# Performance work log

Hardware: AMD Instinct MI355X
Metric: run time of the kernel (lower is better)

The kernel has to match this reference:

```python
import jax, jax.numpy as jnp
import numpy as np

NEG_BIG = -9e15


def setup_inputs() -> dict:
    key = jax.random.key(0)
    k1, k2, k3, k4 = jax.random.split(key, 4)
    B, N, F_in, F_out = 8, 2048, 512, 256
    x = jax.random.normal(k1, (B, N, F_in), dtype=jnp.float32)
    adj = jax.random.randint(k2, (B, N, N), 0, 2, dtype=jnp.int32)
    W = jax.random.normal(k3, (F_in, F_out), dtype=jnp.float32) * (1.414 / np.sqrt(F_in))
    a = jax.random.normal(k4, (2 * F_out, 1), dtype=jnp.float32) * 0.1
    return {"x": x, "adj": adj, "W": W, "a": a}


def reference(x, adj, W, a):
    # x: [B,N,Fin], adj: [B,N,N] int mask, W: [Fin,Fout], a: [2*Fout,1]
    alpha = 0.2  # LeakyReLU negative slope
    F_out = W.shape[1]
    h = jnp.einsum('bnf,fo->bno', x, W)              # [B,N,Fout]
    a1 = a[:F_out, 0]                                # [Fout]
    a2 = a[F_out:, 0]                                # [Fout]
    # e_ij = LeakyReLU([h_i || h_j] . a) = LeakyReLU(h_i.a1 + h_j.a2)
    f = h @ a1                                       # [B,N]
    g = h @ a2                                       # [B,N]
    e = jax.nn.leaky_relu(f[:, :, None] + g[:, None, :], negative_slope=alpha)  # [B,N,N]
    e = jnp.where(adj > 0, e, NEG_BIG)
    attention = jax.nn.softmax(e, axis=2)            # row-wise over neighbors j
    h_prime = jnp.einsum('bij,bjo->bio', attention, h)  # [B,N,Fout]
    return jax.nn.elu(h_prime)                       # concat=True path
```

## Files before the change

### kernel.cpp

```cpp
#include <hip/hip_runtime.h>
#include <math.h>

#define BATCH 8
#define NN    2048
#define FIN   512
#define FOUT  256
#define NEG_BIG -9000000000000000.0f

typedef __attribute__((ext_vector_type(8))) short bf16x8;
typedef __attribute__((ext_vector_type(4))) float f32x4;

__device__ __forceinline__ unsigned short f2bf(float x) {
    unsigned u = __float_as_uint(x);
    u = (u + 0x7FFF + ((u >> 16) & 1)) >> 16;
    return (unsigned short)u;
}
__device__ __forceinline__ float bf2f(unsigned short h) {
    return __uint_as_float(((unsigned)h) << 16);
}
__device__ __forceinline__ void gload_lds16(const void* g, void* l) {
    __builtin_amdgcn_global_load_lds((const __attribute__((address_space(1))) void*)g,
                                     (__attribute__((address_space(3))) void*)l,
                                     16, 0, 0);
}

__global__ __launch_bounds__(256) void wt_prep(const float* __restrict__ W,
                                               unsigned short* __restrict__ Wt_hi,
                                               unsigned short* __restrict__ Wt_lo) {
    const int tg = blockIdx.x * 256 + threadIdx.x;
    const int n  = tg >> 7;
    const int k4 = (tg & 127) * 4;
    unsigned short h[4], lo[4];
    #pragma unroll
    for (int i = 0; i < 4; i++) {
        const float v = W[(size_t)(k4 + i) * FOUT + n];
        h[i]  = f2bf(v);
        lo[i] = f2bf(v - bf2f(h[i]));
    }
    uint2 ph, pl;
    ph.x = h[0]  | ((unsigned)h[1]  << 16); ph.y = h[2]  | ((unsigned)h[3]  << 16);
    pl.x = lo[0] | ((unsigned)lo[1] << 16); pl.y = lo[2] | ((unsigned)lo[3] << 16);
    *(uint2*)(Wt_hi + (size_t)n * FIN + k4) = ph;
    *(uint2*)(Wt_lo + (size_t)n * FIN + k4) = pl;
}

__global__ __launch_bounds__(256, 2) void gemm_xw(const float* __restrict__ x,
        const unsigned short* __restrict__ Wt_hi,
        const unsigned short* __restrict__ Wt_lo,
        unsigned short* __restrict__ ht_hi,
        unsigned short* __restrict__ ht_lo) {
    __shared__ unsigned short As_hi[128][40];
    __shared__ unsigned short As_lo[128][40];
    __shared__ __attribute__((aligned(16))) unsigned short Tr[64][136];
    const int t  = threadIdx.x;
    const int m0 = (blockIdx.x >> 2) * 128;
    const int n0 = (blockIdx.x & 3) * 64;
    const int l  = t & 63, w = t >> 6;
    const int wr = w >> 1, wc = w & 1;
    const int lr = l & 15, lk = l >> 4;

    f32x4 acc[4][2];
    #pragma unroll
    for (int mt = 0; mt < 4; mt++)
        #pragma unroll
        for (int nt = 0; nt < 2; nt++) acc[mt][nt] = (f32x4){0.f,0.f,0.f,0.f};

    for (int k0 = 0; k0 < FIN; k0 += 32) {
        float4 xv[4];
        #pragma unroll
        for (int r = 0; r < 4; r++) {
            const int fidx = t + 256*r, m = fidx >> 3, kq = fidx & 7;
            xv[r] = *(const float4*)(x + (size_t)(m0 + m) * FIN + k0 + kq*4);
        }
        bf16x8 bh[2], bl[2];
        #pragma unroll
        for (int nt = 0; nt < 2; nt++) {
            const size_t off = (size_t)(n0 + wc*32 + nt*16 + lr) * FIN + k0 + lk*8;
            bh[nt] = *(const bf16x8*)(Wt_hi + off);
            bl[nt] = *(const bf16x8*)(Wt_lo + off);
        }
        __syncthreads();
        #pragma unroll
        for (int r = 0; r < 4; r++) {
            const int fidx = t + 256*r, m = fidx >> 3, kq = fidx & 7;
            const float vv[4] = {xv[r].x, xv[r].y, xv[r].z, xv[r].w};
            unsigned short h[4], lo[4];
            #pragma unroll
            for (int i = 0; i < 4; i++) { h[i] = f2bf(vv[i]); lo[i] = f2bf(vv[i] - bf2f(h[i])); }
            uint2 ph, pl;
            ph.x = h[0]  | ((unsigned)h[1]  << 16); ph.y = h[2]  | ((unsigned)h[3]  << 16);
            pl.x = lo[0] | ((unsigned)lo[1] << 16); pl.y = lo[2] | ((unsigned)lo[3] << 16);
            *(uint2*)&As_hi[m][kq*4] = ph;
            *(uint2*)&As_lo[m][kq*4] = pl;
        }
        __syncthreads();
        bf16x8 ah[4], al[4];
        #pragma unroll
        for (int mt = 0; mt < 4; mt++) {
            const int row = wr*64 + mt*16 + lr;
            ah[mt] = *(const bf16x8*)&As_hi[row][lk*8];
            al[mt] = *(const bf16x8*)&As_lo[row][lk*8];
        }
        #pragma unroll
        for (int nt = 0; nt < 2; nt++)
            #pragma unroll
            for (int mt = 0; mt < 4; mt++)
                acc[mt][nt] = __builtin_amdgcn_mfma_f32_16x16x32_bf16(ah[mt], bh[nt], acc[mt][nt], 0, 0, 0);
        #pragma unroll
        for (int nt = 0; nt < 2; nt++)
            #pragma unroll
            for (int mt = 0; mt < 4; mt++)
                acc[mt][nt] = __builtin_amdgcn_mfma_f32_16x16x32_bf16(ah[mt], bl[nt], acc[mt][nt], 0, 0, 0);
        #pragma unroll
        for (int nt = 0; nt < 2; nt++)
            #pragma unroll
            for (int mt = 0; mt < 4; mt++)
                acc[mt][nt] = __builtin_amdgcn_mfma_f32_16x16x32_bf16(al[mt], bh[nt], acc[mt][nt], 0, 0, 0);
    }

    const int bb  = m0 >> 11;
    const int jj0 = m0 & 2047;
    for (int pass = 0; pass < 2; pass++) {
        #pragma unroll
        for (int mt = 0; mt < 4; mt++)
            #pragma unroll
            for (int nt = 0; nt < 2; nt++) {
                const int nl = wc*32 + nt*16 + lr;
                const int ml = wr*64 + mt*16 + lk*4;
                const float vv[4] = {acc[mt][nt].x, acc[mt][nt].y, acc[mt][nt].z, acc[mt][nt].w};
                unsigned short s[4];
                #pragma unroll
                for (int r = 0; r < 4; r++) {
                    const unsigned short hh = f2bf(vv[r]);
                    s[r] = pass ? f2bf(vv[r] - bf2f(hh)) : hh;
                }
                *(unsigned*)&Tr[nl][ml]     = s[0] | ((unsigned)s[1] << 16);
                *(unsigned*)&Tr[nl][ml + 2] = s[2] | ((unsigned)s[3] << 16);
            }
        __syncthreads();
        unsigned short* dst = pass ? ht_lo : ht_hi;
        #pragma unroll
        for (int q = 0; q < 4; q++) {
            const int idx = t + 256*q, row = idx >> 4, c = idx & 15;
            *(uint4*)(dst + ((size_t)(bb * FOUT + n0 + row)) * NN + jj0 + c*8) =
                *(const uint4*)&Tr[row][c*8];
        }
        __syncthreads();
    }
}

__global__ __launch_bounds__(256) void fg2(const unsigned short* __restrict__ ht_hi,
                                           const unsigned short* __restrict__ ht_lo,
                                           const float* __restrict__ a,
                                           float* __restrict__ f, float* __restrict__ g) {
    const int lane  = threadIdx.x & 63;
    const int chunk = blockIdx.x * 4 + (threadIdx.x >> 6);
    const int b  = chunk >> 5;
    const int jw = (chunk & 31) * 64 + lane;
    const size_t base = (size_t)b * FOUT * NN + jw;
    float fs = 0.f, gs = 0.f;
    #pragma unroll 4
    for (int n = 0; n < FOUT; n++) {
        const float hv = bf2f(ht_hi[base + (size_t)n * NN]) + bf2f(ht_lo[base + (size_t)n * NN]);
        fs = fmaf(hv, a[n], fs);
        gs = fmaf(hv, a[FOUT + n], gs);
    }
    f[b * NN + jw] = fs;
    g[b * NN + jw] = gs;
}

__global__ __launch_bounds__(512, 1) void gat_attn(
        const unsigned short* __restrict__ ht_hi,
        const unsigned short* __restrict__ ht_lo,
        const int* __restrict__ adj,
        const float* __restrict__ f, const float* __restrict__ g,
        float* __restrict__ out) {
    __shared__ __attribute__((aligned(16))) unsigned short Hs_hi[256*64];
    __shared__ __attribute__((aligned(16))) unsigned short Hs_lo[256*64];
    __shared__ __attribute__((aligned(16))) unsigned short Ps_hi[64*64];
    __shared__ __attribute__((aligned(16))) unsigned short Ps_lo[64*64];
    __shared__ __attribute__((aligned(16))) float m_s[64];
    __shared__ __attribute__((aligned(16))) float l_s[64];
    __shared__ __attribute__((aligned(16))) float fac_s[64];

    const int b  = blockIdx.x & 7;
    const int i0 = (blockIdx.x >> 3) * 64;
    const int t  = threadIdx.x;
    const int w  = t >> 6, l = t & 63;
    const int lr = l & 15, lk = l >> 4;
    const int wr = w >> 2, wc = w & 3;
    const int ar = t >> 3, jg = t & 7;

    const float fi = f[b * NN + i0 + ar];
    if (t < 64) { m_s[t] = -INFINITY; l_s[t] = 0.f; }

    f32x4 acc[2][4];
    #pragma unroll
    for (int mt = 0; mt < 2; mt++)
        #pragma unroll
        for (int nt = 0; nt < 4; nt++) acc[mt][nt] = (f32x4){0.f,0.f,0.f,0.f};

    const unsigned short* hb_hi = ht_hi + (size_t)b * FOUT * NN;
    const unsigned short* hb_lo = ht_lo + (size_t)b * FOUT * NN;
    const size_t arow = ((size_t)b * NN + i0 + ar) * NN + jg * 8;
    const float* grow = g + b * NN + jg * 8;

    int4   adjA = *(const int4*)(adj + arow);
    int4   adjB = *(const int4*)(adj + arow + 4);
    float4 gA   = *(const float4*)(grow);
    float4 gB   = *(const float4*)(grow + 4);

    const int sidx = w * 4;

    for (int jt = 0; jt < 32; jt++) {
        __syncthreads();

        const int j0 = jt * 64;
        #pragma unroll
        for (int q = 0; q < 4; q++) {
            const int idx = (sidx + q) * 64 + l;
            const int n = idx >> 3, c = idx & 7;
            const int cc = c ^ (n & 7);
            const size_t go = (size_t)n * NN + j0 + cc * 8;
            gload_lds16(hb_hi + go, &Hs_hi[(sidx + q) * 512]);
            gload_lds16(hb_lo + go, &Hs_lo[(sidx + q) * 512]);
        }

        {
            float s[8];
            {
                const float v0 = fi + gA.x, v1 = fi + gA.y, v2 = fi + gA.z, v3 = fi + gA.w;
                const float v4 = fi + gB.x, v5 = fi + gB.y, v6 = fi + gB.z, v7 = fi + gB.w;
                s[0] = adjA.x > 0 ? (v0 > 0.f ? v0 : 0.2f*v0) : NEG_BIG;
                s[1] = adjA.y > 0 ? (v1 > 0.f ? v1 : 0.2f*v1) : NEG_BIG;
                s[2] = adjA.z > 0 ? (v2 > 0.f ? v2 : 0.2f*v2) : NEG_BIG;
                s[3] = adjA.w > 0 ? (v3 > 0.f ? v3 : 0.2f*v3) : NEG_BIG;
                s[4] = adjB.x > 0 ? (v4 > 0.f ? v4 : 0.2f*v4) : NEG_BIG;
                s[5] = adjB.y > 0 ? (v5 > 0.f ? v5 : 0.2f*v5) : NEG_BIG;
                s[6] = adjB.z > 0 ? (v6 > 0.f ? v6 : 0.2f*v6) : NEG_BIG;
                s[7] = adjB.w > 0 ? (v7 > 0.f ? v7 : 0.2f*v7) : NEG_BIG;
            }
            float mloc = s[0];
            #pragma unroll
            for (int e = 1; e < 8; e++) mloc = fmaxf(mloc, s[e]);
            mloc = fmaxf(mloc, __shfl_xor(mloc, 1));
            mloc = fmaxf(mloc, __shfl_xor(mloc, 2));
            mloc = fmaxf(mloc, __shfl_xor(mloc, 4));
            const float m_old = m_s[ar];
            const float m_new = fmaxf(m_old, mloc);
            float p[8], rs = 0.f;
            #pragma unroll
            for (int e = 0; e < 8; e++) { p[e] = __expf(s[e] - m_new); rs += p[e]; }
            rs += __shfl_xor(rs, 1);
            rs += __shfl_xor(rs, 2);
            rs += __shfl_xor(rs, 4);
            if (jg == 0) {
                const float fac = __expf(m_old - m_new);
                fac_s[ar] = fac;
                l_s[ar]   = l_s[ar] * fac + rs;
                m_s[ar]   = m_new;
            }
            unsigned ph[4], pl[4];
            #pragma unroll
            for (int e = 0; e < 8; e += 2) {
                const unsigned short h0 = f2bf(p[e]),   h1 = f2bf(p[e+1]);
                const unsigned short q0 = f2bf(p[e] - bf2f(h0));
                const unsigned short q1 = f2bf(p[e+1] - bf2f(h1));
                ph[e >> 1] = h0 | ((unsigned)h1 << 16);
                pl[e >> 1] = q0 | ((unsigned)q1 << 16);
            }
            const int cs = (jg ^ (ar & 7)) * 8;
            *(uint4*)&Ps_hi[ar * 64 + cs] = make_uint4(ph[0], ph[1], ph[2], ph[3]);
            *(uint4*)&Ps_lo[ar * 64 + cs] = make_uint4(pl[0], pl[1], pl[2], pl[3]);
        }
        __syncthreads();

        if (jt + 1 < 32) {
            const size_t o = (size_t)(jt + 1) * 64;
            adjA = *(const int4*)(adj + arow + o);
            adjB = *(const int4*)(adj + arow + o + 4);
            gA   = *(const float4*)(grow + o);
            gB   = *(const float4*)(grow + o + 4);
        }

        #pragma unroll
        for (int mt = 0; mt < 2; mt++) {
            const f32x4 fac4 = *(const f32x4*)&fac_s[wr*32 + mt*16 + lk*4];
            #pragma unroll
            for (int nt = 0; nt < 4; nt++) acc[mt][nt] *= fac4;
        }
        #pragma unroll
        for (int kt = 0; kt < 2; kt++) {
            bf16x8 ah[2], al[2], bh[4], bl[4];
            #pragma unroll
            for (int mt = 0; mt < 2; mt++) {
                const int row = wr*32 + mt*16 + lr;
                const int cs  = ((kt*4 + lk) ^ (row & 7)) * 8;
                ah[mt] = *(const bf16x8*)&Ps_hi[row * 64 + cs];
                al[mt] = *(const bf16x8*)&Ps_lo[row * 64 + cs];
            }
            #pragma unroll
            for (int nt = 0; nt < 4; nt++) {
                const int n  = wc*64 + nt*16 + lr;
                const int cs = ((kt*4 + lk) ^ (n & 7)) * 8;
                bh[nt] = *(const bf16x8*)&Hs_hi[n * 64 + cs];
                bl[nt] = *(const bf16x8*)&Hs_lo[n * 64 + cs];
            }
            #pragma unroll
            for (int nt = 0; nt < 4; nt++)
                #pragma unroll
                for (int mt = 0; mt < 2; mt++)
                    acc[mt][nt] = __builtin_amdgcn_mfma_f32_16x16x32_bf16(ah[mt], bh[nt], acc[mt][nt], 0, 0, 0);
            #pragma unroll
            for (int nt = 0; nt < 4; nt++)
                #pragma unroll
                for (int mt = 0; mt < 2; mt++)
                    acc[mt][nt] = __builtin_amdgcn_mfma_f32_16x16x32_bf16(ah[mt], bl[nt], acc[mt][nt], 0, 0, 0);
            #pragma unroll
            for (int nt = 0; nt < 4; nt++)
                #pragma unroll
                for (int mt = 0; mt < 2; mt++)
                    acc[mt][nt] = __builtin_amdgcn_mfma_f32_16x16x32_bf16(al[mt], bh[nt], acc[mt][nt], 0, 0, 0);
        }
    }

    __syncthreads();
    #pragma unroll
    for (int mt = 0; mt < 2; mt++) {
        const f32x4 lv = *(const f32x4*)&l_s[wr*32 + mt*16 + lk*4];
        const float linv[4] = {1.f/lv.x, 1.f/lv.y, 1.f/lv.z, 1.f/lv.w};
        #pragma unroll
        for (int nt = 0; nt < 4; nt++) {
            const int n = wc*64 + nt*16 + lr;
            const float av[4] = {acc[mt][nt].x, acc[mt][nt].y, acc[mt][nt].z, acc[mt][nt].w};
            #pragma unroll
            for (int r = 0; r < 4; r++) {
                float v = av[r] * linv[r];
                v = v > 0.f ? v : (__expf(v) - 1.f);
                out[((size_t)(b * NN + i0 + wr*32 + mt*16 + lk*4 + r)) * FOUT + n] = v;
            }
        }
    }
}

extern "C" void kernel_launch(void* const* d_in, const int* in_sizes, int n_in,
                              void* d_out, int out_size, void* d_ws, size_t ws_size,
                              hipStream_t stream) {
    const float* x   = (const float*)d_in[0];
    const int*   adj = (const int*)  d_in[1];
    const float* W   = (const float*)d_in[2];
    const float* a   = (const float*)d_in[3];
    float* outp = (float*)d_out;

    char* ws = (char*)d_ws;
    unsigned short* ht_hi = (unsigned short*)ws;                       ws += (size_t)BATCH*FOUT*NN*2;
    unsigned short* ht_lo = (unsigned short*)ws;                       ws += (size_t)BATCH*FOUT*NN*2;
    unsigned short* Wt_hi = (unsigned short*)ws;                       ws += (size_t)FOUT*FIN*2;
    unsigned short* Wt_lo = (unsigned short*)ws;                       ws += (size_t)FOUT*FIN*2;
    float* f = (float*)ws;                                             ws += (size_t)BATCH*NN*4;
    float* g = (float*)ws;

    wt_prep <<<128, 256, 0, stream>>>(W, Wt_hi, Wt_lo);
    gemm_xw <<<512, 256, 0, stream>>>(x, Wt_hi, Wt_lo, ht_hi, ht_lo);
    fg2     <<<64,  256, 0, stream>>>(ht_hi, ht_lo, a, f, g);
    gat_attn<<<256, 512, 0, stream>>>(ht_hi, ht_lo, adj, f, g, outp);
}
```

Before: 320.5 us.

## Double-buffer H tiles in attention, pre-swizzle W to fragment layout, split fg2 reduction

The attention kernel now keeps the H tiles in two LDS buffers and issues the next tile's async global-to-LDS loads before the softmax of the current tile. It keeps the running max and sum in registers instead of shared memory, uses custom lgkmcnt barriers, and raises wave priority around the MFMA block. W is pre-arranged in MFMA fragment order so gemm_xw reads it with contiguous per-lane loads. fg2 splits the feature reduction across four waves and launches four times as many blocks. Each change targets latency hiding or load efficiency, at the cost of twice the H-tile LDS footprint and more complex synchronization.

```diff
diff --git a/kernel.cpp b/kernel.cpp
--- a/kernel.cpp
+++ b/kernel.cpp
@@ -1,4 +1,5 @@
 #include <hip/hip_runtime.h>
+#include <hip/hip_bf16.h>
 #include <math.h>
 
 #define BATCH 8
@@ -11,9 +12,7 @@
 typedef __attribute__((ext_vector_type(4))) float f32x4;
 
 __device__ __forceinline__ unsigned short f2bf(float x) {
-    unsigned u = __float_as_uint(x);
-    u = (u + 0x7FFF + ((u >> 16) & 1)) >> 16;
-    return (unsigned short)u;
+    return __bfloat16_as_ushort(__float2bfloat16(x));
 }
 __device__ __forceinline__ float bf2f(unsigned short h) {
     return __uint_as_float(((unsigned)h) << 16);
@@ -23,10 +22,15 @@
                                      (__attribute__((address_space(3))) void*)l,
                                      16, 0, 0);
 }
+__device__ __forceinline__ void lds_barrier() {
+    asm volatile("s_waitcnt lgkmcnt(0)" ::: "memory");
+    __builtin_amdgcn_s_barrier();
+    asm volatile("" ::: "memory");
+}
 
 __global__ __launch_bounds__(256) void wt_prep(const float* __restrict__ W,
-                                               unsigned short* __restrict__ Wt_hi,
-                                               unsigned short* __restrict__ Wt_lo) {
+                                               unsigned short* __restrict__ Wtf_hi,
+                                               unsigned short* __restrict__ Wtf_lo) {
     const int tg = blockIdx.x * 256 + threadIdx.x;
     const int n  = tg >> 7;
     const int k4 = (tg & 127) * 4;
@@ -37,16 +41,20 @@
         h[i]  = f2bf(v);
         lo[i] = f2bf(v - bf2f(h[i]));
     }
+    const int ktile = k4 >> 5;
+    const int ntile = n >> 4;
+    const int lane  = ((k4 >> 3) & 3) * 16 + (n & 15);
+    const size_t daddr = ((size_t)(ktile * 16 + ntile) * 64 + lane) * 8 + (k4 & 7);
     uint2 ph, pl;
     ph.x = h[0]  | ((unsigned)h[1]  << 16); ph.y = h[2]  | ((unsigned)h[3]  << 16);
     pl.x = lo[0] | ((unsigned)lo[1] << 16); pl.y = lo[2] | ((unsigned)lo[3] << 16);
-    *(uint2*)(Wt_hi + (size_t)n * FIN + k4) = ph;
-    *(uint2*)(Wt_lo + (size_t)n * FIN + k4) = pl;
+    *(uint2*)(Wtf_hi + daddr) = ph;
+    *(uint2*)(Wtf_lo + daddr) = pl;
 }
 
 __global__ __launch_bounds__(256, 2) void gemm_xw(const float* __restrict__ x,
-        const unsigned short* __restrict__ Wt_hi,
-        const unsigned short* __restrict__ Wt_lo,
+        const unsigned short* __restrict__ Wtf_hi,
+        const unsigned short* __restrict__ Wtf_lo,
         unsigned short* __restrict__ ht_hi,
         unsigned short* __restrict__ ht_lo) {
     __shared__ unsigned short As_hi[128][40];
@@ -73,11 +81,11 @@
             xv[r] = *(const float4*)(x + (size_t)(m0 + m) * FIN + k0 + kq*4);
         }
         bf16x8 bh[2], bl[2];
+        const size_t fb = ((size_t)((k0 >> 5) * 16 + (n0 >> 4) + wc*2) * 64 + l) * 8;
         #pragma unroll
         for (int nt = 0; nt < 2; nt++) {
-            const size_t off = (size_t)(n0 + wc*32 + nt*16 + lr) * FIN + k0 + lk*8;
-            bh[nt] = *(const bf16x8*)(Wt_hi + off);
-            bl[nt] = *(const bf16x8*)(Wt_lo + off);
+            bh[nt] = *(const bf16x8*)(Wtf_hi + fb + (size_t)nt * 512);
+            bl[nt] = *(const bf16x8*)(Wtf_lo + fb + (size_t)nt * 512);
         }
         __syncthreads();
         #pragma unroll
@@ -153,20 +161,25 @@
                                            const unsigned short* __restrict__ ht_lo,
                                            const float* __restrict__ a,
                                            float* __restrict__ f, float* __restrict__ g) {
-    const int lane  = threadIdx.x & 63;
-    const int chunk = blockIdx.x * 4 + (threadIdx.x >> 6);
+    __shared__ float Fp[4][64], Gp[4][64];
+    const int lane = threadIdx.x & 63, wv = threadIdx.x >> 6;
+    const int chunk = blockIdx.x;
     const int b  = chunk >> 5;
     const int jw = (chunk & 31) * 64 + lane;
     const size_t base = (size_t)b * FOUT * NN + jw;
     float fs = 0.f, gs = 0.f;
     #pragma unroll 4
-    for (int n = 0; n < FOUT; n++) {
+    for (int n = wv*64; n < wv*64 + 64; n++) {
         const float hv = bf2f(ht_hi[base + (size_t)n * NN]) + bf2f(ht_lo[base + (size_t)n * NN]);
         fs = fmaf(hv, a[n], fs);
         gs = fmaf(hv, a[FOUT + n], gs);
     }
-    f[b * NN + jw] = fs;
-    g[b * NN + jw] = gs;
+    Fp[wv][lane] = fs; Gp[wv][lane] = gs;
+    __syncthreads();
+    if (wv == 0) {
+        f[b * NN + jw] = Fp[0][lane] + Fp[1][lane] + Fp[2][lane] + Fp[3][lane];
+        g[b * NN + jw] = Gp[0][lane] + Gp[1][lane] + Gp[2][lane] + Gp[3][lane];
+    }
 }
 
 __global__ __launch_bounds__(512, 1) void gat_attn(
@@ -175,13 +188,12 @@
         const int* __restrict__ adj,
         const float* __restrict__ f, const float* __restrict__ g,
         float* __restrict__ out) {
-    __shared__ __attribute__((aligned(16))) unsigned short Hs_hi[256*64];
-    __shared__ __attribute__((aligned(16))) unsigned short Hs_lo[256*64];
-    __shared__ __attribute__((aligned(16))) unsigned short Ps_hi[64*64];
-    __shared__ __attribute__((aligned(16))) unsigned short Ps_lo[64*64];
-    __shared__ __attribute__((aligned(16))) float m_s[64];
+    __shared__ __attribute__((aligned(16))) unsigned short Hs_hi[2][16384];
+    __shared__ __attribute__((aligned(16))) unsigned short Hs_lo[2][16384];
+    __shared__ __attribute__((aligned(16))) unsigned short Ps_hi[4096];
+    __shared__ __attribute__((aligned(16))) unsigned short Ps_lo[4096];
+    __shared__ __attribute__((aligned(16))) float fac_s[64];
     __shared__ __attribute__((aligned(16))) float l_s[64];
-    __shared__ __attribute__((aligned(16))) float fac_s[64];
 
     const int b  = blockIdx.x & 7;
     const int i0 = (blockIdx.x >> 3) * 64;
@@ -191,97 +203,95 @@
     const int wr = w >> 2, wc = w & 3;
     const int ar = t >> 3, jg = t & 7;
 
-    const float fi = f[b * NN + i0 + ar];
-    if (t < 64) { m_s[t] = -INFINITY; l_s[t] = 0.f; }
-
-    f32x4 acc[2][4];
-    #pragma unroll
-    for (int mt = 0; mt < 2; mt++)
-        #pragma unroll
-        for (int nt = 0; nt < 4; nt++) acc[mt][nt] = (f32x4){0.f,0.f,0.f,0.f};
-
     const unsigned short* hb_hi = ht_hi + (size_t)b * FOUT * NN;
     const unsigned short* hb_lo = ht_lo + (size_t)b * FOUT * NN;
-    const size_t arow = ((size_t)b * NN + i0 + ar) * NN + jg * 8;
-    const float* grow = g + b * NN + jg * 8;
-
-    int4   adjA = *(const int4*)(adj + arow);
-    int4   adjB = *(const int4*)(adj + arow + 4);
-    float4 gA   = *(const float4*)(grow);
-    float4 gB   = *(const float4*)(grow + 4);
-
-    const int sidx = w * 4;
-
-    for (int jt = 0; jt < 32; jt++) {
-        __syncthreads();
-
-        const int j0 = jt * 64;
+    const int*   adjr = adj + ((size_t)(b * NN + i0 + ar)) * NN + jg * 8;
+    const float* gb   = g + b * NN + jg * 8;
+    const float  fi   = f[b * NN + i0 + ar];
+
+    float m_r = -INFINITY, l_r = 0.f;
+    f32x4 acc[2][4] = {};
+    const int slot = w * 4;
+
+    int4 a0v, a1v; float4 g0v, g1v;
+
+    auto STAGE = [&](int jt) {
+        const int buf = jt & 1, j0 = jt * 64;
         #pragma unroll
         for (int q = 0; q < 4; q++) {
-            const int idx = (sidx + q) * 64 + l;
+            const int idx = (slot + q) * 64 + l;
             const int n = idx >> 3, c = idx & 7;
             const int cc = c ^ (n & 7);
             const size_t go = (size_t)n * NN + j0 + cc * 8;
-            gload_lds16(hb_hi + go, &Hs_hi[(sidx + q) * 512]);
-            gload_lds16(hb_lo + go, &Hs_lo[(sidx + q) * 512]);
-        }
+            gload_lds16(hb_hi + go, &Hs_hi[buf][(slot + q) * 512]);
+            gload_lds16(hb_lo + go, &Hs_lo[buf][(slot + q) * 512]);
+        }
+    };
+    auto LOADAG = [&](int jt) {
+        const size_t jo = (size_t)jt * 64;
+        a0v = *(const int4*)(adjr + jo);
+        a1v = *(const int4*)(adjr + jo + 4);
+        g0v = *(const float4*)(gb + jo);
+        g1v = *(const float4*)(gb + jo + 4);
+    };
+
+    STAGE(0);
+    asm volatile("" ::: "memory");
+    LOADAG(0);
+
+    for (int jt = 0; jt < 32; jt++) {
+        const int buf = jt & 1;
+        if (jt + 1 < 32) STAGE(jt + 1);
+        asm volatile("" ::: "memory");
 
         {
-            float s[8];
+            float p[8];
             {
-                const float v0 = fi + gA.x, v1 = fi + gA.y, v2 = fi + gA.z, v3 = fi + gA.w;
-                const float v4 = fi + gB.x, v5 = fi + gB.y, v6 = fi + gB.z, v7 = fi + gB.w;
-                s[0] = adjA.x > 0 ? (v0 > 0.f ? v0 : 0.2f*v0) : NEG_BIG;
-                s[1] = adjA.y > 0 ? (v1 > 0.f ? v1 : 0.2f*v1) : NEG_BIG;
-                s[2] = adjA.z > 0 ? (v2 > 0.f ? v2 : 0.2f*v2) : NEG_BIG;
-                s[3] = adjA.w > 0 ? (v3 > 0.f ? v3 : 0.2f*v3) : NEG_BIG;
-                s[4] = adjB.x > 0 ? (v4 > 0.f ? v4 : 0.2f*v4) : NEG_BIG;
-                s[5] = adjB.y > 0 ? (v5 > 0.f ? v5 : 0.2f*v5) : NEG_BIG;
-                s[6] = adjB.z > 0 ? (v6 > 0.f ? v6 : 0.2f*v6) : NEG_BIG;
-                s[7] = adjB.w > 0 ? (v7 > 0.f ? v7 : 0.2f*v7) : NEG_BIG;
-            }
-            float mloc = s[0];
-            #pragma unroll
-            for (int e = 1; e < 8; e++) mloc = fmaxf(mloc, s[e]);
+                const float v0 = fi + g0v.x, v1 = fi + g0v.y, v2 = fi + g0v.z, v3 = fi + g0v.w;
+                const float v4 = fi + g1v.x, v5 = fi + g1v.y, v6 = fi + g1v.z, v7 = fi + g1v.w;
+                p[0] = a0v.x > 0 ? (v0 > 0.f ? v0 : 0.2f*v0) : NEG_BIG;
+                p[1] = a0v.y > 0 ? (v1 > 0.f ? v1 : 0.2f*v1) : NEG_BIG;
+                p[2] = a0v.z > 0 ? (v2 > 0.f ? v2 : 0.2f*v2) : NEG_BIG;
+                p[3] = a0v.w > 0 ? (v3 > 0.f ? v3 : 0.2f*v3) : NEG_BIG;
+                p[4] = a1v.x > 0 ? (v4 > 0.f ? v4 : 0.2f*v4) : NEG_BIG;
+                p[5] = a1v.y > 0 ? (v5 > 0.f ? v5 : 0.2f*v5) : NEG_BIG;
+                p[6] = a1v.z > 0 ? (v6 > 0.f ? v6 : 0.2f*v6) : NEG_BIG;
+                p[7] = a1v.w > 0 ? (v7 > 0.f ? v7 : 0.2f*v7) : NEG_BIG;
+            }
+            float mloc = p[0];
+            #pragma unroll
+            for (int e = 1; e < 8; e++) mloc = fmaxf(mloc, p[e]);
             mloc = fmaxf(mloc, __shfl_xor(mloc, 1));
             mloc = fmaxf(mloc, __shfl_xor(mloc, 2));
             mloc = fmaxf(mloc, __shfl_xor(mloc, 4));
-            const float m_old = m_s[ar];
-            const float m_new = fmaxf(m_old, mloc);
-            float p[8], rs = 0.f;
-            #pragma unroll
-            for (int e = 0; e < 8; e++) { p[e] = __expf(s[e] - m_new); rs += p[e]; }
+            const float mn = fmaxf(m_r, mloc);
+            float rs = 0.f;
+            #pragma unroll
+            for (int e = 0; e < 8; e++) { p[e] = __expf(p[e] - mn); rs += p[e]; }
             rs += __shfl_xor(rs, 1);
             rs += __shfl_xor(rs, 2);
             rs += __shfl_xor(rs, 4);
-            if (jg == 0) {
-                const float fac = __expf(m_old - m_new);
-                fac_s[ar] = fac;
-                l_s[ar]   = l_s[ar] * fac + rs;
-                m_s[ar]   = m_new;
-            }
-            unsigned ph[4], pl[4];
+            const float fac = __expf(m_r - mn);
+            l_r = l_r * fac + rs;
+            m_r = mn;
+            if (jg == 0) { fac_s[ar] = fac; l_s[ar] = l_r; }
+            unsigned hw_[4], lw_[4];
             #pragma unroll
             for (int e = 0; e < 8; e += 2) {
                 const unsigned short h0 = f2bf(p[e]),   h1 = f2bf(p[e+1]);
-                const unsigned short q0 = f2bf(p[e] - bf2f(h0));
+                const unsigned short q0 = f2bf(p[e]   - bf2f(h0));
                 const unsigned short q1 = f2bf(p[e+1] - bf2f(h1));
-                ph[e >> 1] = h0 | ((unsigned)h1 << 16);
-                pl[e >> 1] = q0 | ((unsigned)q1 << 16);
+                hw_[e >> 1] = h0 | ((unsigned)h1 << 16);
+                lw_[e >> 1] = q0 | ((unsigned)q1 << 16);
             }
             const int cs = (jg ^ (ar & 7)) * 8;
-            *(uint4*)&Ps_hi[ar * 64 + cs] = make_uint4(ph[0], ph[1], ph[2], ph[3]);
-            *(uint4*)&Ps_lo[ar * 64 + cs] = make_uint4(pl[0], pl[1], pl[2], pl[3]);
-        }
-        __syncthreads();
-
-        if (jt + 1 < 32) {
-            const size_t o = (size_t)(jt + 1) * 64;
-            adjA = *(const int4*)(adj + arow + o);
-            adjB = *(const int4*)(adj + arow + o + 4);
-            gA   = *(const float4*)(grow + o);
-            gB   = *(const float4*)(grow + o + 4);
-        }
+            *(uint4*)&Ps_hi[ar * 64 + cs] = make_uint4(hw_[0], hw_[1], hw_[2], hw_[3]);
+            *(uint4*)&Ps_lo[ar * 64 + cs] = make_uint4(lw_[0], lw_[1], lw_[2], lw_[3]);
+        }
+
+        if (jt + 1 < 32) LOADAG(jt + 1);
+
+        lds_barrier();
 
         #pragma unroll
         for (int mt = 0; mt < 2; mt++) {
@@ -289,6 +299,7 @@
             #pragma unroll
             for (int nt = 0; nt < 4; nt++) acc[mt][nt] *= fac4;
         }
+        __builtin_amdgcn_s_setprio(1);
         #pragma unroll
         for (int kt = 0; kt < 2; kt++) {
             bf16x8 ah[2], al[2], bh[4], bl[4];
@@ -303,8 +314,8 @@
             for (int nt = 0; nt < 4; nt++) {
                 const int n  = wc*64 + nt*16 + lr;
                 const int cs = ((kt*4 + lk) ^ (n & 7)) * 8;
-                bh[nt] = *(const bf16x8*)&Hs_hi[n * 64 + cs];
-                bl[nt] = *(const bf16x8*)&Hs_lo[n * 64 + cs];
+                bh[nt] = *(const bf16x8*)&Hs_hi[buf][n * 64 + cs];
+                bl[nt] = *(const bf16x8*)&Hs_lo[buf][n * 64 + cs];
             }
             #pragma unroll
             for (int nt = 0; nt < 4; nt++)
@@ -322,20 +333,22 @@
                 for (int mt = 0; mt < 2; mt++)
                     acc[mt][nt] = __builtin_amdgcn_mfma_f32_16x16x32_bf16(al[mt], bh[nt], acc[mt][nt], 0, 0, 0);
         }
-    }
-
-    __syncthreads();
+        __builtin_amdgcn_s_setprio(0);
+
+        lds_barrier();
+    }
+
     #pragma unroll
     for (int mt = 0; mt < 2; mt++) {
         const f32x4 lv = *(const f32x4*)&l_s[wr*32 + mt*16 + lk*4];
-        const float linv[4] = {1.f/lv.x, 1.f/lv.y, 1.f/lv.z, 1.f/lv.w};
+        const float li[4] = {1.f/lv.x, 1.f/lv.y, 1.f/lv.z, 1.f/lv.w};
         #pragma unroll
         for (int nt = 0; nt < 4; nt++) {
             const int n = wc*64 + nt*16 + lr;
             const float av[4] = {acc[mt][nt].x, acc[mt][nt].y, acc[mt][nt].z, acc[mt][nt].w};
             #pragma unroll
             for (int r = 0; r < 4; r++) {
-                float v = av[r] * linv[r];
+                float v = av[r] * li[r];
                 v = v > 0.f ? v : (__expf(v) - 1.f);
                 out[((size_t)(b * NN + i0 + wr*32 + mt*16 + lk*4 + r)) * FOUT + n] = v;
             }
@@ -353,15 +366,15 @@
     float* outp = (float*)d_out;
 
     char* ws = (char*)d_ws;
-    unsigned short* ht_hi = (unsigned short*)ws;                       ws += (size_t)BATCH*FOUT*NN*2;
-    unsigned short* ht_lo = (unsigned short*)ws;                       ws += (size_t)BATCH*FOUT*NN*2;
-    unsigned short* Wt_hi = (unsigned short*)ws;                       ws += (size_t)FOUT*FIN*2;
-    unsigned short* Wt_lo = (unsigned short*)ws;                       ws += (size_t)FOUT*FIN*2;
+    unsigned short* ht_hi  = (unsigned short*)ws;                      ws += (size_t)BATCH*FOUT*NN*2;
+    unsigned short* ht_lo  = (unsigned short*)ws;                      ws += (size_t)BATCH*FOUT*NN*2;
+    unsigned short* Wtf_hi = (unsigned short*)ws;                      ws += (size_t)FOUT*FIN*2;
+    unsigned short* Wtf_lo = (unsigned short*)ws;                      ws += (size_t)FOUT*FIN*2;
     float* f = (float*)ws;                                             ws += (size_t)BATCH*NN*4;
     float* g = (float*)ws;
 
-    wt_prep <<<128, 256, 0, stream>>>(W, Wt_hi, Wt_lo);
-    gemm_xw <<<512, 256, 0, stream>>>(x, Wt_hi, Wt_lo, ht_hi, ht_lo);
-    fg2     <<<64,  256, 0, stream>>>(ht_hi, ht_lo, a, f, g);
+    wt_prep <<<128, 256, 0, stream>>>(W, Wtf_hi, Wtf_lo);
+    gemm_xw <<<512, 256, 0, stream>>>(x, Wtf_hi, Wtf_lo, ht_hi, ht_lo);
+    fg2     <<<256, 256, 0, stream>>>(ht_hi, ht_lo, a, f, g);
     gat_attn<<<256, 512, 0, stream>>>(ht_hi, ht_lo, adj, f, g, outp);
 }
```

After: 287.3 us. 10.3% less time.
